# Kernel optimization log

Hardware: AMD Instinct MI355X
Metric: run time of the kernel (lower is better)

The kernel has to match this reference:

```python
import jax, jax.numpy as jnp
import numpy as np

HEATMAPS_LOSS_FACTOR = 1.0
PUSH_LOSS_FACTOR = 0.001
PULL_LOSS_FACTOR = 0.001

B, K, H, W, M = 16, 17, 256, 256, 30  # batch, joints, heatmap HxW, max people
N = K * H * W  # flattened tag length per image


def setup_inputs() -> dict:
    key = jax.random.key(0)
    k1, k2, k3, k4, k5, k6 = jax.random.split(key, 6)
    heatmaps_pred = jax.random.normal(k1, (B, K, H, W), dtype=jnp.float32)
    heatmaps = jax.random.uniform(k2, (B, K, H, W), dtype=jnp.float32)
    masks = (jax.random.uniform(k3, (B, K, H, W)) > 0.1).astype(jnp.float32)
    tags_pred = jax.random.normal(k4, (B, K, H, W), dtype=jnp.float32)
    idx = jax.random.randint(k5, (B, M, K), 0, N)
    vis = jax.random.randint(k6, (B, M, K), 0, 2)  # ~half joints visible
    joints = jnp.stack([idx, vis], axis=-1).astype(jnp.int32)
    return {
        "heatmaps_pred": heatmaps_pred,
        "heatmaps": heatmaps,
        "masks": masks,
        "tags_pred": tags_pred,
        "joints": joints,
    }


def _single_tag_loss(tag_flat, joints_img):
    # tag_flat: [N], joints_img: [M, K, 2] (flat index, visibility)
    idx = joints_img[..., 0]                      # [M, K]
    vis = (joints_img[..., 1] > 0)                # [M, K] bool
    visf = vis.astype(tag_flat.dtype)
    t = tag_flat[idx]                             # [M, K] gathered tags
    cnt = jnp.sum(visf, axis=-1)                  # [M] visible joints per person
    person_valid = cnt > 0                        # [M]
    safe_cnt = jnp.maximum(cnt, 1.0)
    mu = jnp.sum(t * visf, axis=-1) / safe_cnt    # [M] per-person mean tag
    pull_pp = jnp.sum(visf * (t - mu[:, None]) ** 2, axis=-1) / safe_cnt  # [M]
    n = jnp.sum(person_valid.astype(tag_flat.dtype))  # num_tags
    pull = jnp.sum(jnp.where(person_valid, pull_pp, 0.0)) / jnp.maximum(n, 1.0)
    # push: pairwise exp(-(mu_i - mu_j)^2) over valid persons; diagonal sums to n
    diff = mu[:, None] - mu[None, :]              # [M, M]
    pair_mask = person_valid[:, None] & person_valid[None, :]
    s = jnp.sum(jnp.where(pair_mask, jnp.exp(-(diff ** 2)), 0.0))
    denom = jnp.maximum((n - 1.0) * n, 1.0)
    push = jnp.where(n >= 2.0, (s - n) / denom * 0.5, 0.0)
    return push, pull


def reference(heatmaps_pred, heatmaps, masks, tags_pred, joints):
    # HeatmapLoss: mean over all dims of (pred - gt)^2 * mask
    heatmaps_loss = jnp.mean((heatmaps_pred - heatmaps) ** 2 * masks)
    heatmaps_loss = heatmaps_loss * HEATMAPS_LOSS_FACTOR
    # AELoss over flattened tag maps, vectorized across the batch
    b = tags_pred.shape[0]
    tag_flat = tags_pred.reshape(b, -1)           # [B, N]
    push, pull = jax.vmap(_single_tag_loss)(tag_flat, joints)
    push_loss = jnp.mean(push) * PUSH_LOSS_FACTOR
    pull_loss = jnp.mean(pull) * PULL_LOSS_FACTOR
    return (heatmaps_loss, push_loss, pull_loss)
```

## Files before the change

### kernel.cpp

```cpp
#include <hip/hip_runtime.h>

#define Bn 16
#define Kn 17
#define Hn 256
#define Wn 256
#define Mn 30
#define NFLAT (Kn * Hn * Wn)
#define TOTAL ((long long)Bn * Kn * Hn * Wn)
#define NVEC  (TOTAL / 4)

#define HEAT_BLOCKS 2048
#define HEAT_THREADS 256

__global__ __launch_bounds__(HEAT_THREADS) void heat_partial_kernel(
    const float4* __restrict__ pred,
    const float4* __restrict__ gt,
    const float4* __restrict__ mask,
    float* __restrict__ partial, int nvec) {
    float acc = 0.f;
    int stride = gridDim.x * blockDim.x;
    for (int i = blockIdx.x * blockDim.x + threadIdx.x; i < nvec; i += stride) {
        float4 p = pred[i];
        float4 g = gt[i];
        float4 m = mask[i];
        float dx = p.x - g.x, dy = p.y - g.y, dz = p.z - g.z, dw = p.w - g.w;
        acc += dx * dx * m.x + dy * dy * m.y + dz * dz * m.z + dw * dw * m.w;
    }
    __shared__ float s[HEAT_THREADS];
    s[threadIdx.x] = acc;
    __syncthreads();
    for (int off = HEAT_THREADS / 2; off > 0; off >>= 1) {
        if (threadIdx.x < off) s[threadIdx.x] += s[threadIdx.x + off];
        __syncthreads();
    }
    if (threadIdx.x == 0) partial[blockIdx.x] = s[0];
}

__global__ __launch_bounds__(64) void ae_kernel(
    const float* __restrict__ tags,
    const int* __restrict__ joints,
    float* __restrict__ out_push,
    float* __restrict__ out_pull) {
    int b = blockIdx.x;
    int lane = threadIdx.x;

    __shared__ float s_mu[Mn];
    __shared__ float s_valid[Mn];

    float mu = 0.f, pullpp = 0.f, validf = 0.f;
    if (lane < Mn) {
        const int* jb = joints + ((long long)(b * Mn + lane) * Kn) * 2;
        const float* tb = tags + (long long)b * NFLAT;
        float t[Kn];
        float v[Kn];
        float cnt = 0.f, st = 0.f;
#pragma unroll
        for (int k = 0; k < Kn; k++) {
            int id = jb[2 * k];
            int vi = jb[2 * k + 1];
            float tv = tb[id];
            t[k] = tv;
            v[k] = (vi > 0) ? 1.f : 0.f;
            cnt += v[k];
            st += v[k] * tv;
        }
        float sc = fmaxf(cnt, 1.f);
        mu = st / sc;
        float pp = 0.f;
#pragma unroll
        for (int k = 0; k < Kn; k++) {
            float d = t[k] - mu;
            pp += v[k] * d * d;
        }
        pullpp = pp / sc;
        validf = (cnt > 0.f) ? 1.f : 0.f;
        s_mu[lane] = mu;
        s_valid[lane] = validf;
    }
    __syncthreads();

    float nv = validf;
    float pv = (validf > 0.f) ? pullpp : 0.f;
    float sm = 0.f;
    if (lane < Mn && validf > 0.f) {
        for (int j = 0; j < Mn; j++) {
            if (s_valid[j] > 0.f) {
                float d = mu - s_mu[j];
                sm += expf(-(d * d));
            }
        }
    }
    for (int off = 32; off > 0; off >>= 1) {
        nv += __shfl_down(nv, off, 64);
        pv += __shfl_down(pv, off, 64);
        sm += __shfl_down(sm, off, 64);
    }
    if (lane == 0) {
        float n = nv;
        float pull = pv / fmaxf(n, 1.f);
        float denom = fmaxf((n - 1.f) * n, 1.f);
        float push = (n >= 2.f) ? (sm - n) / denom * 0.5f : 0.f;
        out_push[b] = push;
        out_pull[b] = pull;
    }
}

__global__ __launch_bounds__(256) void finalize_kernel(
    const float* __restrict__ partial, int nblocks,
    const float* __restrict__ push_arr,
    const float* __restrict__ pull_arr,
    float* __restrict__ out) {
    __shared__ double sd[256];
    double acc = 0.0;
    for (int i = threadIdx.x; i < nblocks; i += 256) acc += (double)partial[i];
    sd[threadIdx.x] = acc;
    __syncthreads();
    for (int off = 128; off > 0; off >>= 1) {
        if (threadIdx.x < off) sd[threadIdx.x] += sd[threadIdx.x + off];
        __syncthreads();
    }
    if (threadIdx.x == 0) {
        double heat = sd[0] / (double)TOTAL;
        float psum = 0.f, lsum = 0.f;
        for (int b = 0; b < Bn; b++) {
            psum += push_arr[b];
            lsum += pull_arr[b];
        }
        out[0] = (float)heat;
        out[1] = (psum / (float)Bn) * 0.001f;
        out[2] = (lsum / (float)Bn) * 0.001f;
    }
}

extern "C" void kernel_launch(void* const* d_in, const int* in_sizes, int n_in,
                              void* d_out, int out_size, void* d_ws, size_t ws_size,
                              hipStream_t stream) {
    const float* heatmaps_pred = (const float*)d_in[0];
    const float* heatmaps      = (const float*)d_in[1];
    const float* masks         = (const float*)d_in[2];
    const float* tags_pred     = (const float*)d_in[3];
    const int*   joints        = (const int*)d_in[4];
    float* out = (float*)d_out;

    float* ws = (float*)d_ws;
    float* partial  = ws;
    float* push_arr = ws + HEAT_BLOCKS;
    float* pull_arr = push_arr + Bn;

    heat_partial_kernel<<<HEAT_BLOCKS, HEAT_THREADS, 0, stream>>>(
        (const float4*)heatmaps_pred, (const float4*)heatmaps,
        (const float4*)masks, partial, (int)NVEC);

    ae_kernel<<<Bn, 64, 0, stream>>>(tags_pred, joints, push_arr, pull_arr);

    finalize_kernel<<<1, 256, 0, stream>>>(partial, HEAT_BLOCKS,
                                           push_arr, pull_arr, out);
}
```

Baseline: 46.63 us.

## Fuse heatmap reduction and AE loss into one kernel with extra blocks

```diff
diff --git a/kernel.cpp b/kernel.cpp
--- a/kernel.cpp
+++ b/kernel.cpp
@@ -7,101 +7,107 @@
 #define Mn 30
 #define NFLAT (Kn * Hn * Wn)
 #define TOTAL ((long long)Bn * Kn * Hn * Wn)
-#define NVEC  (TOTAL / 4)
+#define NVEC  ((int)(TOTAL / 4))
+#define NPAIR (NVEC / 2)
 
 #define HEAT_BLOCKS 2048
-#define HEAT_THREADS 256
+#define THREADS 256
+#define AE_BLOCKS Bn
 
-__global__ __launch_bounds__(HEAT_THREADS) void heat_partial_kernel(
+__global__ __launch_bounds__(THREADS) void fused_kernel(
     const float4* __restrict__ pred,
     const float4* __restrict__ gt,
     const float4* __restrict__ mask,
-    float* __restrict__ partial, int nvec) {
-    float acc = 0.f;
-    int stride = gridDim.x * blockDim.x;
-    for (int i = blockIdx.x * blockDim.x + threadIdx.x; i < nvec; i += stride) {
-        float4 p = pred[i];
-        float4 g = gt[i];
-        float4 m = mask[i];
-        float dx = p.x - g.x, dy = p.y - g.y, dz = p.z - g.z, dw = p.w - g.w;
-        acc += dx * dx * m.x + dy * dy * m.y + dz * dz * m.z + dw * dw * m.w;
-    }
-    __shared__ float s[HEAT_THREADS];
-    s[threadIdx.x] = acc;
-    __syncthreads();
-    for (int off = HEAT_THREADS / 2; off > 0; off >>= 1) {
-        if (threadIdx.x < off) s[threadIdx.x] += s[threadIdx.x + off];
-        __syncthreads();
-    }
-    if (threadIdx.x == 0) partial[blockIdx.x] = s[0];
-}
-
-__global__ __launch_bounds__(64) void ae_kernel(
     const float* __restrict__ tags,
     const int* __restrict__ joints,
-    float* __restrict__ out_push,
-    float* __restrict__ out_pull) {
-    int b = blockIdx.x;
-    int lane = threadIdx.x;
+    float* __restrict__ partial,
+    float* __restrict__ push_arr,
+    float* __restrict__ pull_arr) {
+    __shared__ float smem[64];
 
-    __shared__ float s_mu[Mn];
-    __shared__ float s_valid[Mn];
+    if (blockIdx.x < HEAT_BLOCKS) {
+        int tid = blockIdx.x * THREADS + threadIdx.x;
+        const int stride = HEAT_BLOCKS * THREADS;
+        float acc0 = 0.f, acc1 = 0.f;
+        for (int i = tid; i < NPAIR; i += stride) {
+            float4 p0 = pred[2 * i], p1 = pred[2 * i + 1];
+            float4 g0 = gt[2 * i],   g1 = gt[2 * i + 1];
+            float4 m0 = mask[2 * i], m1 = mask[2 * i + 1];
+            float dx, dy, dz, dw;
+            dx = p0.x - g0.x; dy = p0.y - g0.y; dz = p0.z - g0.z; dw = p0.w - g0.w;
+            acc0 += dx * dx * m0.x + dy * dy * m0.y + dz * dz * m0.z + dw * dw * m0.w;
+            dx = p1.x - g1.x; dy = p1.y - g1.y; dz = p1.z - g1.z; dw = p1.w - g1.w;
+            acc1 += dx * dx * m1.x + dy * dy * m1.y + dz * dz * m1.z + dw * dw * m1.w;
+        }
+        float a = acc0 + acc1;
+        for (int off = 32; off > 0; off >>= 1) a += __shfl_down(a, off, 64);
+        int wave = threadIdx.x >> 6;
+        if ((threadIdx.x & 63) == 0) smem[wave] = a;
+        __syncthreads();
+        if (threadIdx.x == 0)
+            partial[blockIdx.x] = smem[0] + smem[1] + smem[2] + smem[3];
+    } else {
+        int b = blockIdx.x - HEAT_BLOCKS;
+        int lane = threadIdx.x;
 
-    float mu = 0.f, pullpp = 0.f, validf = 0.f;
-    if (lane < Mn) {
-        const int* jb = joints + ((long long)(b * Mn + lane) * Kn) * 2;
-        const float* tb = tags + (long long)b * NFLAT;
-        float t[Kn];
-        float v[Kn];
-        float cnt = 0.f, st = 0.f;
+        float mu = 0.f, pullpp = 0.f, validf = 0.f;
+        if (lane < Mn) {
+            const int* jb = joints + ((long long)(b * Mn + lane) * Kn) * 2;
+            const float* tb = tags + (long long)b * NFLAT;
+            float t[Kn], v[Kn];
+            float cnt = 0.f, st = 0.f;
 #pragma unroll
-        for (int k = 0; k < Kn; k++) {
-            int id = jb[2 * k];
-            int vi = jb[2 * k + 1];
-            float tv = tb[id];
-            t[k] = tv;
-            v[k] = (vi > 0) ? 1.f : 0.f;
-            cnt += v[k];
-            st += v[k] * tv;
+            for (int k = 0; k < Kn; k++) {
+                int id = jb[2 * k];
+                int vi = jb[2 * k + 1];
+                float tv = tb[id];
+                t[k] = tv;
+                v[k] = (vi > 0) ? 1.f : 0.f;
+                cnt += v[k];
+                st += v[k] * tv;
+            }
+            float sc = fmaxf(cnt, 1.f);
+            mu = st / sc;
+            float pp = 0.f;
+#pragma unroll
+            for (int k = 0; k < Kn; k++) {
+                float d = t[k] - mu;
+                pp += v[k] * d * d;
+            }
+            pullpp = pp / sc;
+            validf = (cnt > 0.f) ? 1.f : 0.f;
+            smem[lane] = mu;
+            smem[32 + lane] = validf;
         }
-        float sc = fmaxf(cnt, 1.f);
-        mu = st / sc;
-        float pp = 0.f;
-#pragma unroll
-        for (int k = 0; k < Kn; k++) {
-            float d = t[k] - mu;
-            pp += v[k] * d * d;
-        }
-        pullpp = pp / sc;
-        validf = (cnt > 0.f) ? 1.f : 0.f;
-        s_mu[lane] = mu;
-        s_valid[lane] = validf;
-    }
-    __syncthreads();
+        __syncthreads();
 
-    float nv = validf;
-    float pv = (validf > 0.f) ? pullpp : 0.f;
-    float sm = 0.f;
-    if (lane < Mn && validf > 0.f) {
-        for (int j = 0; j < Mn; j++) {
-            if (s_valid[j] > 0.f) {
-                float d = mu - s_mu[j];
-                sm += expf(-(d * d));
+        if (lane < 64) {
+            float nv = validf;
+            float pv = (validf > 0.f) ? pullpp : 0.f;
+            float sm = 0.f;
+            if (lane < Mn && validf > 0.f) {
+                for (int j = 0; j < Mn; j++) {
+                    if (smem[32 + j] > 0.f) {
+                        float d = mu - smem[j];
+                        sm += expf(-(d * d));
+                    }
+                }
+            }
+            for (int off = 32; off > 0; off >>= 1) {
+                nv += __shfl_down(nv, off, 64);
+                pv += __shfl_down(pv, off, 64);
+                sm += __shfl_down(sm, off, 64);
+            }
+            if (lane == 0) {
+                float n = nv;
+                float pull = pv / fmaxf(n, 1.f);
+                float denom = fmaxf((n - 1.f) * n, 1.f);
+                float push = (n >= 2.f) ? (sm - n) / denom * 0.5f : 0.f;
+                out_push:
+                push_arr[b] = push;
+                pull_arr[b] = pull;
             }
         }
-    }
-    for (int off = 32; off > 0; off >>= 1) {
-        nv += __shfl_down(nv, off, 64);
-        pv += __shfl_down(pv, off, 64);
-        sm += __shfl_down(sm, off, 64);
-    }
-    if (lane == 0) {
-        float n = nv;
-        float pull = pv / fmaxf(n, 1.f);
-        float denom = fmaxf((n - 1.f) * n, 1.f);
-        float push = (n >= 2.f) ? (sm - n) / denom * 0.5f : 0.f;
-        out_push[b] = push;
-        out_pull[b] = pull;
     }
 }
 
@@ -147,11 +153,9 @@
     float* push_arr = ws + HEAT_BLOCKS;
     float* pull_arr = push_arr + Bn;
 
-    heat_partial_kernel<<<HEAT_BLOCKS, HEAT_THREADS, 0, stream>>>(
+    fused_kernel<<<HEAT_BLOCKS + AE_BLOCKS, THREADS, 0, stream>>>(
         (const float4*)heatmaps_pred, (const float4*)heatmaps,
-        (const float4*)masks, partial, (int)NVEC);
-
-    ae_kernel<<<Bn, 64, 0, stream>>>(tags_pred, joints, push_arr, pull_arr);
+        (const float4*)masks, tags_pred, joints, partial, push_arr, pull_arr);
 
     finalize_kernel<<<1, 256, 0, stream>>>(partial, HEAT_BLOCKS,
                                            push_arr, pull_arr, out);
```

Result: faster. 40.84 us (-12.4%).
